# Kernel optimization log

Hardware: AMD Instinct MI355X
Metric: run time of the kernel (lower is better)

The kernel has to match this reference:

```python
import jax, jax.numpy as jnp
import numpy as np

BN_EPS = 1e-5
NN_EPS = 1e-8


def _three_nn_interp(xyz1, xyz2, points2):
    # xyz1: [B,N,3], xyz2: [B,S,3], points2: [B,S,D]
    # squared pairwise distances [B,N,S]
    d = (jnp.sum(xyz1 ** 2, -1)[:, :, None]
         + jnp.sum(xyz2 ** 2, -1)[:, None, :]
         - 2.0 * jnp.einsum('bnc,bsc->bns', xyz1, xyz2))
    neg_d3, idx = jax.lax.top_k(-d, 3)          # top-3 smallest dists
    d3 = -neg_d3                                # [B,N,3]
    recip = 1.0 / (d3 + NN_EPS)
    weight = recip / jnp.sum(recip, axis=2, keepdims=True)  # [B,N,3]
    gathered = jax.vmap(lambda p, i: p[i])(points2, idx)    # [B,N,3,D]
    return jnp.sum(gathered * weight[..., None], axis=2)    # [B,N,D]


def _conv_bn_relu(x, w, b, gamma, beta):
    # x: [B,C,N]; 1x1 conv == channel GEMM; BN in training mode (batch stats)
    y = jnp.einsum('oc,bcn->bon', w, x) + b[None, :, None]
    mean = jnp.mean(y, axis=(0, 2), keepdims=True)
    var = jnp.mean((y - mean) ** 2, axis=(0, 2), keepdims=True)
    y = (y - mean) * jax.lax.rsqrt(var + BN_EPS)
    y = y * gamma[None, :, None] + beta[None, :, None]
    return jax.nn.relu(y)


def setup_inputs() -> dict:
    key = jax.random.key(0)
    ks = jax.random.split(key, 8)
    B, N, S, D1, D2 = 8, 8192, 2048, 256, 256
    Cin, C0, C1 = D1 + D2, 256, 256
    return {
        'xyz1': jax.random.normal(ks[0], (B, 3, N), jnp.float32),
        'xyz2': jax.random.normal(ks[1], (B, 3, S), jnp.float32),
        'points1': jax.random.normal(ks[2], (B, D1, N), jnp.float32),
        'points2': jax.random.normal(ks[3], (B, D2, S), jnp.float32),
        'w0': jax.random.normal(ks[4], (C0, Cin), jnp.float32) * (1.0 / np.sqrt(Cin)),
        'b0': jnp.zeros((C0,), jnp.float32),
        'gamma0': jnp.ones((C0,), jnp.float32),
        'beta0': jnp.zeros((C0,), jnp.float32),
        'w1': jax.random.normal(ks[5], (C1, C0), jnp.float32) * (1.0 / np.sqrt(C0)),
        'b1': jnp.zeros((C1,), jnp.float32),
        'gamma1': jnp.ones((C1,), jnp.float32),
        'beta1': jnp.zeros((C1,), jnp.float32),
    }


def reference(xyz1, xyz2, points1, points2, w0, b0, gamma0, beta0, w1, b1, gamma1, beta1):
    x1 = jnp.transpose(xyz1, (0, 2, 1))     # [B,N,3]
    x2 = jnp.transpose(xyz2, (0, 2, 1))     # [B,S,3]
    p2 = jnp.transpose(points2, (0, 2, 1))  # [B,S,D2]
    interp = _three_nn_interp(x1, x2, p2)   # [B,N,D2]
    p1 = jnp.transpose(points1, (0, 2, 1))  # [B,N,D1]
    new_points = jnp.transpose(jnp.concatenate([p1, interp], axis=-1), (0, 2, 1))  # [B,Cin,N]
    h = _conv_bn_relu(new_points, w0, b0, gamma0, beta0)
    return _conv_bn_relu(h, w1, b1, gamma1, beta1)
```

## Files before the change

### kernel.cpp

```cpp
#include <hip/hip_runtime.h>
#include <math.h>

#define B 8
#define N 8192
#define S 2048
#define SCH 1024
#define C 256
#define CIN 512
#define CNT (B * N)
#define NSLOT 1024

typedef unsigned long long ull;
typedef __attribute__((ext_vector_type(8))) short bf16x8;
typedef __attribute__((ext_vector_type(4))) float floatx4;
typedef __attribute__((ext_vector_type(8))) unsigned short ushort8v;
typedef __attribute__((ext_vector_type(4))) unsigned short ushort4v;

__device__ inline unsigned short f2bf(float f) {
  unsigned u = __builtin_bit_cast(unsigned, f);
  u += 0x7FFF + ((u >> 16) & 1);
  return (unsigned short)(u >> 16);
}
__device__ inline float bf2f(unsigned short h) {
  unsigned u = ((unsigned)h) << 16;
  return __builtin_bit_cast(float, u);
}

__device__ inline void load_lds16(const void* g, void* l) {
  __builtin_amdgcn_global_load_lds(
      (const __attribute__((address_space(1))) unsigned int*)g,
      (__attribute__((address_space(3))) unsigned int*)l, 16, 0, 0);
}

__device__ inline void ins3u(ull k, ull& k0, ull& k1, ull& k2) {
  if (k < k2) {
    if (k < k1) {
      k2 = k1;
      if (k < k0) { k1 = k0; k0 = k; } else k1 = k;
    } else k2 = k;
  }
}

__device__ inline unsigned sortkey(float f) {
  unsigned u = __float_as_uint(f);
  return u ^ (((unsigned)((int)u >> 31)) | 0x80000000u);
}
__device__ inline float unsortkey(unsigned u) {
  unsigned m = ((int)u < 0) ? 0x80000000u : 0xFFFFFFFFu;
  return __uint_as_float(u ^ m);
}

__device__ inline void out3q(ull k0, ull k1, ull k2, float q2v,
                             int* __restrict__ idxbuf, float* __restrict__ wbuf,
                             size_t o) {
  float e0 = fmaxf(unsortkey((unsigned)(k0 >> 32)) + q2v, 0.0f);
  float e1 = fmaxf(unsortkey((unsigned)(k1 >> 32)) + q2v, 0.0f);
  float e2 = fmaxf(unsortkey((unsigned)(k2 >> 32)) + q2v, 0.0f);
  float r0 = 1.0f / (e0 + 1e-8f);
  float r1 = 1.0f / (e1 + 1e-8f);
  float r2 = 1.0f / (e2 + 1e-8f);
  float rs = 1.0f / (r0 + r1 + r2);
  idxbuf[o] = (int)(unsigned)k0;
  idxbuf[o + 1] = (int)(unsigned)k1;
  idxbuf[o + 2] = (int)(unsigned)k2;
  wbuf[o] = r0 * rs; wbuf[o + 1] = r1 * rs; wbuf[o + 2] = r2 * rs;
}

#define QDECL(q)                                                            \
  float d0_##q = INFINITY, d1_##q = INFINITY, d2_##q = INFINITY;            \
  int i0_##q = 0, i1_##q = 0, i2_##q = 0;                                   \
  float qx_##q, qy_##q, qz_##q, q2_##q;

#define QLOAD(q)                                                            \
  {                                                                         \
    float ox = p1[nq + q], oy = p1[N + nq + q], oz = p1[2 * N + nq + q];    \
    q2_##q = ox * ox + oy * oy + oz * oz;                                   \
    qx_##q = -2.0f * ox; qy_##q = -2.0f * oy; qz_##q = -2.0f * oz;          \
  }

#define QINS(q)                                                             \
  {                                                                         \
    float d = fmaf(qx_##q, pc.x, fmaf(qy_##q, pc.y, fmaf(qz_##q, pc.z, pc.w))); \
    bool lt0 = d < d0_##q, lt1 = d < d1_##q, lt2 = d < d2_##q;              \
    i2_##q = lt2 ? (lt1 ? i1_##q : s) : i2_##q;                             \
    i1_##q = lt1 ? (lt0 ? i0_##q : s) : i1_##q;                             \
    i0_##q = lt0 ? s : i0_##q;                                              \
    d2_##q = __builtin_amdgcn_fmed3f(d, d1_##q, d2_##q);                    \
    d1_##q = __builtin_amdgcn_fmed3f(d, d0_##q, d1_##q);                    \
    d0_##q = fminf(d, d0_##q);                                              \
  }

#define QSTORE(q)                                                           \
  {                                                                         \
    size_t kb = ((size_t)(grp * 2 + q) * 16 + sub) * 3;                     \
    keys[kb] = ((ull)sortkey(d0_##q) << 32) | (unsigned)i0_##q;             \
    keys[kb + 1] = ((ull)sortkey(d1_##q) << 32) | (unsigned)i1_##q;         \
    keys[kb + 2] = ((ull)sortkey(d2_##q) << 32) | (unsigned)i2_##q;         \
  }

__global__ __launch_bounds__(256, 4) void nn3_kernel(const float* __restrict__ xyz1,
                                                     const float* __restrict__ xyz2,
                                                     int* __restrict__ idxbuf,
                                                     float* __restrict__ wbuf) {
  __shared__ float4 sp[SCH];
  int b = blockIdx.x >> 8;
  int n0 = (blockIdx.x & 255) * 32;
  const float* p2 = xyz2 + (size_t)b * 3 * S;
  int tid = threadIdx.x;
  int sub = tid & 15, grp = tid >> 4;
  const float* p1 = xyz1 + (size_t)b * 3 * N;
  int nq = n0 + grp * 2;
  QDECL(0) QDECL(1)
  QLOAD(0) QLOAD(1)

  for (int ch = 0; ch < 2; ++ch) {
    if (ch) __syncthreads();
    for (int i = tid; i < SCH; i += 256) {
      int g = ch * SCH + i;
      float px = p2[g], py = p2[S + g], pz = p2[2 * S + g];
      sp[i] = make_float4(px, py, pz, px * px + py * py + pz * pz);
    }
    __syncthreads();
    int sbase = ch * SCH;
    float4 pc = sp[sub];
    for (int t = 0; t < SCH / 16 - 1; ++t) {
      float4 pn = sp[(t + 1) * 16 + sub];
      int s = sbase + t * 16 + sub;
      QINS(0) QINS(1)
      pc = pn;
    }
    {
      int s = sbase + SCH - 16 + sub;
      QINS(0) QINS(1)
    }
  }

  __syncthreads();
  ull* keys = (ull*)sp;
  QSTORE(0) QSTORE(1)
  __syncthreads();
  if (sub < 4) {
#pragma unroll
    for (int q = 0; q < 2; ++q) {
      size_t qb = (size_t)(grp * 2 + q) * 48;
      ull m0 = ~0ull, m1 = ~0ull, m2 = ~0ull;
#pragma unroll
      for (int jj = 0; jj < 4; ++jj) {
        size_t o2 = qb + (size_t)(sub + 4 * jj) * 3;
        ins3u(keys[o2], m0, m1, m2);
        ins3u(keys[o2 + 1], m0, m1, m2);
        ins3u(keys[o2 + 2], m0, m1, m2);
      }
#pragma unroll
      for (int mm = 1; mm <= 2; mm <<= 1) {
        ull e0 = (ull)__shfl_xor((long long)m0, mm);
        ull e1 = (ull)__shfl_xor((long long)m1, mm);
        ull e2 = (ull)__shfl_xor((long long)m2, mm);
        ins3u(e0, m0, m1, m2);
        ins3u(e1, m0, m1, m2);
        ins3u(e2, m0, m1, m2);
      }
      if (sub == 0) {
        float q2v = q ? q2_1 : q2_0;
        out3q(m0, m1, m2, q2v, idxbuf, wbuf, ((size_t)b * N + nq + q) * 3);
      }
    }
  }
}

__global__ __launch_bounds__(256) void convw_kernel(const float* __restrict__ w0,
                                                    const float* __restrict__ w1,
                                                    unsigned short* __restrict__ w0b,
                                                    unsigned short* __restrict__ w1b) {
  int i = blockIdx.x * 256 + threadIdx.x;
  if (i < C * CIN) w0b[i] = f2bf(w0[i]);
  else {
    int j = i - C * CIN;
    if (j < C * C) w1b[j] = f2bf(w1[j]);
  }
}

__global__ __launch_bounds__(256) void tconv_kernel(const float* __restrict__ src,
                                                    unsigned short* __restrict__ dst,
                                                    int cols, int drow, int coff) {
  __shared__ float t[64][65];
  int n0 = blockIdx.x * 64, c0 = blockIdx.y * 64, b = blockIdx.z;
  int tid = threadIdx.x, r = tid >> 2, q = tid & 3;
  const float* sp = src + ((size_t)b * 256 + c0 + r) * cols + n0 + q * 16;
#pragma unroll
  for (int i = 0; i < 4; ++i) {
    float4 v = *(const float4*)(sp + i * 4);
    t[r][q * 16 + i * 4 + 0] = v.x;
    t[r][q * 16 + i * 4 + 1] = v.y;
    t[r][q * 16 + i * 4 + 2] = v.z;
    t[r][q * 16 + i * 4 + 3] = v.w;
  }
  __syncthreads();
  unsigned short* dp = dst + ((size_t)b * cols + n0 + r) * drow + coff + c0 + q * 16;
  ushort8v o0, o1;
#pragma unroll
  for (int i = 0; i < 8; ++i) o0[i] = f2bf(t[q * 16 + i][r]);
#pragma unroll
  for (int i = 0; i < 8; ++i) o1[i] = f2bf(t[q * 16 + 8 + i][r]);
  *(ushort8v*)dp = o0;
  *(ushort8v*)(dp + 8) = o1;
}

__global__ __launch_bounds__(256) void gather_kernel(const unsigned short* __restrict__ p2t,
                                                     const int* __restrict__ idxbuf,
                                                     const float* __restrict__ wbuf,
                                                     unsigned short* __restrict__ Xb) {
  __shared__ int si[192];
  __shared__ float sw[192];
  int b = blockIdx.x >> 7;
  int n0 = (blockIdx.x & 127) * 64;
  size_t base = ((size_t)b * N + n0) * 3;
  if (threadIdx.x < 192) {
    si[threadIdx.x] = idxbuf[base + threadIdx.x];
    sw[threadIdx.x] = wbuf[base + threadIdx.x];
  }
  __syncthreads();
  int nl = threadIdx.x >> 2, cb = threadIdx.x & 3;
  int j0 = si[nl * 3], j1 = si[nl * 3 + 1], j2 = si[nl * 3 + 2];
  float w0 = sw[nl * 3], w1 = sw[nl * 3 + 1], w2 = sw[nl * 3 + 2];
  const unsigned short* pb = p2t + (size_t)b * S * 256;
  const unsigned short* r0p = pb + (size_t)j0 * 256;
  const unsigned short* r1p = pb + (size_t)j1 * 256;
  const unsigned short* r2p = pb + (size_t)j2 * 256;
  unsigned short* xp = Xb + ((size_t)b * N + n0 + nl) * 512 + 256;
#pragma unroll
  for (int ch = 0; ch < 8; ++ch) {
    int co = (cb + ch * 4) * 8;
    ushort8v v0 = *(const ushort8v*)(r0p + co);
    ushort8v v1 = *(const ushort8v*)(r1p + co);
    ushort8v v2 = *(const ushort8v*)(r2p + co);
    ushort8v o;
#pragma unroll
    for (int i = 0; i < 8; ++i)
      o[i] = f2bf(w0 * bf2f(v0[i]) + w1 * bf2f(v1[i]) + w2 * bf2f(v2[i]));
    *(ushort8v*)(xp + co) = o;
  }
}

__global__ __launch_bounds__(256) void gemm_kernel(const unsigned short* __restrict__ X,
                                                   const unsigned short* __restrict__ Wb,
                                                   const float* __restrict__ bias,
                                                   unsigned short* __restrict__ Y,
                                                   float* __restrict__ psum,
                                                   float* __restrict__ psumsq,
                                                   int Cin) {
  __shared__ unsigned short As[128 * 32];
  __shared__ unsigned short Bs[128 * 32];
  int n0 = blockIdx.x * 128, o0 = blockIdx.y * 128, b = blockIdx.z;
  int tid = threadIdx.x, lane = tid & 63, wid = tid >> 6;
  int wm = wid >> 1, wn = wid & 1;
  floatx4 acc[4][4];
#pragma unroll
  for (int m = 0; m < 4; ++m)
#pragma unroll
    for (int nt = 0; nt < 4; ++nt) acc[m][nt] = (floatx4)(0.0f);

  size_t rsA = (size_t)Cin * 2;
  int chunkSwz = ((lane & 3) ^ ((lane >> 3) & 3)) * 16;
  const char* Abase = (const char*)Wb + (size_t)(o0 + wid * 32 + (lane >> 2)) * rsA + chunkSwz;
  const char* Bbase = (const char*)X + ((size_t)b * N + n0 + wid * 32 + (lane >> 2)) * rsA + chunkSwz;
  size_t rstep16 = 16 * rsA;
  int kq = (((lane >> 4) ^ ((lane >> 1) & 3))) * 8;

  for (int k0 = 0; k0 < Cin; k0 += 32) {
    load_lds16(Abase + (size_t)k0 * 2, &As[(wid * 32) * 32]);
    load_lds16(Abase + (size_t)k0 * 2 + rstep16, &As[(wid * 32 + 16) * 32]);
    load_lds16(Bbase + (size_t)k0 * 2, &Bs[(wid * 32) * 32]);
    load_lds16(Bbase + (size_t)k0 * 2 + rstep16, &Bs[(wid * 32 + 16) * 32]);
    __syncthreads();
    bf16x8 af[4], bfv[4];
#pragma unroll
    for (int m = 0; m < 4; ++m)
      af[m] = *(const bf16x8*)&As[(wm * 64 + m * 16 + (lane & 15)) * 32 + kq];
#pragma unroll
    for (int nt = 0; nt < 4; ++nt)
      bfv[nt] = *(const bf16x8*)&Bs[(wn * 64 + nt * 16 + (lane & 15)) * 32 + kq];
#pragma unroll
    for (int m = 0; m < 4; ++m)
#pragma unroll
      for (int nt = 0; nt < 4; ++nt)
        acc[m][nt] = __builtin_amdgcn_mfma_f32_16x16x32_bf16(af[m], bfv[nt], acc[m][nt], 0, 0, 0);
    __syncthreads();
  }

  int col = lane & 15, rowq = lane >> 4;
  int slot = ((b * 64 + blockIdx.x) * 2) + wn;
#pragma unroll
  for (int m = 0; m < 4; ++m) {
    int ob = o0 + wm * 64 + m * 16 + rowq * 4;
    float4 bs = *(const float4*)&bias[ob];
    float sj[4] = {0.f, 0.f, 0.f, 0.f}, qj[4] = {0.f, 0.f, 0.f, 0.f};
#pragma unroll
    for (int nt = 0; nt < 4; ++nt) {
      int n = n0 + wn * 64 + nt * 16 + col;
      float y0 = acc[m][nt][0] + bs.x;
      float y1 = acc[m][nt][1] + bs.y;
      float y2 = acc[m][nt][2] + bs.z;
      float y3 = acc[m][nt][3] + bs.w;
      ushort4v v;
      v[0] = f2bf(y0); v[1] = f2bf(y1); v[2] = f2bf(y2); v[3] = f2bf(y3);
      *(ushort4v*)&Y[((size_t)b * N + n) * 256 + ob] = v;
      sj[0] += y0; qj[0] = fmaf(y0, y0, qj[0]);
      sj[1] += y1; qj[1] = fmaf(y1, y1, qj[1]);
      sj[2] += y2; qj[2] = fmaf(y2, y2, qj[2]);
      sj[3] += y3; qj[3] = fmaf(y3, y3, qj[3]);
    }
#pragma unroll
    for (int j = 0; j < 4; ++j) {
#pragma unroll
      for (int d = 1; d <= 8; d <<= 1) {
        sj[j] += __shfl_xor(sj[j], d);
        qj[j] += __shfl_xor(qj[j], d);
      }
    }
    if (col == 0) {
      int c0 = blockIdx.y * 128 + wm * 64 + m * 16 + rowq * 4;
#pragma unroll
      for (int j = 0; j < 4; ++j) {
        psum[(size_t)(c0 + j) * NSLOT + slot] = sj[j];
        psumsq[(size_t)(c0 + j) * NSLOT + slot] = qj[j];
      }
    }
  }
}

__global__ __launch_bounds__(256) void bnparam_kernel(const float* __restrict__ psum,
                                                      const float* __restrict__ psumsq,
                                                      const float* __restrict__ gamma,
                                                      const float* __restrict__ beta,
                                                      float* __restrict__ scale,
                                                      float* __restrict__ shift) {
  int c = blockIdx.x, tid = threadIdx.x;
  const float* ps = psum + (size_t)c * NSLOT;
  const float* pq = psumsq + (size_t)c * NSLOT;
  float s = 0.f, q = 0.f;
#pragma unroll
  for (int i = 0; i < NSLOT / 256; ++i) {
    s += ps[tid + i * 256];
    q += pq[tid + i * 256];
  }
#pragma unroll
  for (int d = 1; d <= 32; d <<= 1) {
    s += __shfl_xor(s, d);
    q += __shfl_xor(q, d);
  }
  __shared__ float ls[4], lq[4];
  int wid = tid >> 6;
  if ((tid & 63) == 0) { ls[wid] = s; lq[wid] = q; }
  __syncthreads();
  if (tid == 0) {
    s = ls[0] + ls[1] + ls[2] + ls[3];
    q = lq[0] + lq[1] + lq[2] + lq[3];
    float m = s * (1.0f / CNT);
    float v = q * (1.0f / CNT) - m * m;
    float sc = gamma[c] * rsqrtf(v + 1e-5f);
    scale[c] = sc;
    shift[c] = beta[c] - m * sc;
  }
}

__global__ __launch_bounds__(256) void bnrelu_kernel(const unsigned short* __restrict__ Y,
                                                     const float* __restrict__ scale,
                                                     const float* __restrict__ shift,
                                                     unsigned short* __restrict__ H) {
  size_t total = (size_t)B * N * 256 / 8;
  for (size_t i = (size_t)blockIdx.x * 256 + threadIdx.x; i < total;
       i += (size_t)gridDim.x * 256) {
    int ob = ((int)i & 31) * 8;
    float4 s0 = *(const float4*)&scale[ob];
    float4 s1 = *(const float4*)&scale[ob + 4];
    float4 h0 = *(const float4*)&shift[ob];
    float4 h1 = *(const float4*)&shift[ob + 4];
    ushort8v v = *(const ushort8v*)&Y[i * 8];
    ushort8v o;
    o[0] = f2bf(fmaxf(fmaf(bf2f(v[0]), s0.x, h0.x), 0.f));
    o[1] = f2bf(fmaxf(fmaf(bf2f(v[1]), s0.y, h0.y), 0.f));
    o[2] = f2bf(fmaxf(fmaf(bf2f(v[2]), s0.z, h0.z), 0.f));
    o[3] = f2bf(fmaxf(fmaf(bf2f(v[3]), s0.w, h0.w), 0.f));
    o[4] = f2bf(fmaxf(fmaf(bf2f(v[4]), s1.x, h1.x), 0.f));
    o[5] = f2bf(fmaxf(fmaf(bf2f(v[5]), s1.y, h1.y), 0.f));
    o[6] = f2bf(fmaxf(fmaf(bf2f(v[6]), s1.z, h1.z), 0.f));
    o[7] = f2bf(fmaxf(fmaf(bf2f(v[7]), s1.w, h1.w), 0.f));
    *(ushort8v*)&H[i * 8] = o;
  }
}

__global__ __launch_bounds__(256) void bnreluT_kernel(const unsigned short* __restrict__ Y,
                                                      const float* __restrict__ scale,
                                                      const float* __restrict__ shift,
                                                      float* __restrict__ out) {
  __shared__ float t[64][65];
  int n0 = blockIdx.x * 64, o0 = blockIdx.y * 64, b = blockIdx.z;
  int tid = threadIdx.x, r = tid >> 2, q = tid & 3;
  const unsigned short* yp = Y + ((size_t)b * N + n0 + r) * 256 + o0 + q * 16;
#pragma unroll
  for (int h = 0; h < 2; ++h) {
    ushort8v v = *(const ushort8v*)(yp + h * 8);
#pragma unroll
    for (int i = 0; i < 8; ++i) {
      int oc = q * 16 + h * 8 + i;
      float f = fmaxf(fmaf(bf2f(v[i]), scale[o0 + oc], shift[o0 + oc]), 0.f);
      t[oc][r] = f;
    }
  }
  __syncthreads();
  float* op = out + ((size_t)b * 256 + o0 + r) * N + n0 + q * 16;
#pragma unroll
  for (int i = 0; i < 4; ++i) {
    float4 v = make_float4(t[r][q * 16 + i * 4 + 0], t[r][q * 16 + i * 4 + 1],
                           t[r][q * 16 + i * 4 + 2], t[r][q * 16 + i * 4 + 3]);
    *(float4*)(op + i * 4) = v;
  }
}

extern "C" void kernel_launch(void* const* d_in, const int* in_sizes, int n_in,
                              void* d_out, int out_size, void* d_ws, size_t ws_size,
                              hipStream_t stream) {
  const float* xyz1 = (const float*)d_in[0];
  const float* xyz2 = (const float*)d_in[1];
  const float* points1 = (const float*)d_in[2];
  const float* points2 = (const float*)d_in[3];
  const float* w0 = (const float*)d_in[4];
  const float* b0 = (const float*)d_in[5];
  const float* g0 = (const float*)d_in[6];
  const float* be0 = (const float*)d_in[7];
  const float* w1 = (const float*)d_in[8];
  const float* b1 = (const float*)d_in[9];
  const float* g1 = (const float*)d_in[10];
  const float* be1 = (const float*)d_in[11];
  float* out = (float*)d_out;

  char* ws = (char*)d_ws;
  int* idxbuf = (int*)ws;              ws += (size_t)CNT * 3 * 4;
  float* wbuf = (float*)ws;            ws += (size_t)CNT * 3 * 4;
  float* scale0 = (float*)ws;          ws += 256 * 4;
  float* shift0 = (float*)ws;          ws += 256 * 4;
  float* scale1 = (float*)ws;          ws += 256 * 4;
  float* shift1 = (float*)ws;          ws += 256 * 4;
  float* psum = (float*)ws;            ws += (size_t)C * NSLOT * 4;
  float* psumsq = (float*)ws;          ws += (size_t)C * NSLOT * 4;
  unsigned short* w0b = (unsigned short*)ws;  ws += (size_t)C * CIN * 2;
  unsigned short* w1b = (unsigned short*)ws;  ws += (size_t)C * C * 2;
  unsigned short* p2t = (unsigned short*)ws;  ws += (size_t)B * S * 256 * 2;
  unsigned short* Xb = (unsigned short*)ws;   ws += (size_t)B * N * 512 * 2;
  unsigned short* Yb = (unsigned short*)ws;   ws += (size_t)B * N * 256 * 2;
  unsigned short* Hb = Xb;

  convw_kernel<<<dim3((C * CIN + C * C) / 256), 256, 0, stream>>>(w0, w1, w0b, w1b);
  tconv_kernel<<<dim3(N / 64, 4, B), 256, 0, stream>>>(points1, Xb, N, 512, 0);
  tconv_kernel<<<dim3(S / 64, 4, B), 256, 0, stream>>>(points2, p2t, S, 256, 0);
  nn3_kernel<<<dim3(B * N / 32), 256, 0, stream>>>(xyz1, xyz2, idxbuf, wbuf);
  gather_kernel<<<dim3(B * N / 64), 256, 0, stream>>>(p2t, idxbuf, wbuf, Xb);
  gemm_kernel<<<dim3(N / 128, 2, B), 256, 0, stream>>>(Xb, w0b, b0, Yb, psum, psumsq, CIN);
  bnparam_kernel<<<dim3(C), 256, 0, stream>>>(psum, psumsq, g0, be0, scale0, shift0);
  bnrelu_kernel<<<dim3(2048), 256, 0, stream>>>(Yb, scale0, shift0, Hb);
  gemm_kernel<<<dim3(N / 128, 2, B), 256, 0, stream>>>(Hb, w1b, b1, Yb, psum, psumsq, C);
  bnparam_kernel<<<dim3(C), 256, 0, stream>>>(psum, psumsq, g1, be1, scale1, shift1);
  bnreluT_kernel<<<dim3(N / 64, 4, B), 256, 0, stream>>>(Yb, scale1, shift1, out);
}
```

Baseline: 229.9 us.

## Merge prep kernels into one launch and unroll NN candidate loop by two

The weight conversion kernel and the two transpose-convert kernels become a single prep kernel that dispatches on block index, saving two launches and letting their blocks share the GPU. Separately, the three-nearest-neighbour scan loop is unrolled by two, with two LDS candidates prefetched per iteration, to expose more instruction-level parallelism. The unroll raises register pressure in nn3, and the merged kernel must route block indices correctly.

```diff
diff --git a/kernel.cpp b/kernel.cpp
--- a/kernel.cpp
+++ b/kernel.cpp
@@ -122,15 +122,33 @@
     }
     __syncthreads();
     int sbase = ch * SCH;
-    float4 pc = sp[sub];
-    for (int t = 0; t < SCH / 16 - 1; ++t) {
-      float4 pn = sp[(t + 1) * 16 + sub];
-      int s = sbase + t * 16 + sub;
+    const float4* spp = sp + sub;
+    float4 pcA = spp[0];
+    float4 pcB = spp[16];
+    for (int t = 0; t < SCH / 16 - 2; t += 2) {
+      float4 pnA = spp[(t + 2) * 16];
+      float4 pnB = spp[(t + 3) * 16];
+      {
+        float4 pc = pcA;
+        int s = sbase + t * 16 + sub;
+        QINS(0) QINS(1)
+      }
+      {
+        float4 pc = pcB;
+        int s = sbase + (t + 1) * 16 + sub;
+        QINS(0) QINS(1)
+      }
+      pcA = pnA;
+      pcB = pnB;
+    }
+    {
+      float4 pc = pcA;
+      int s = sbase + (SCH / 16 - 2) * 16 + sub;
       QINS(0) QINS(1)
-      pc = pn;
     }
     {
-      int s = sbase + SCH - 16 + sub;
+      float4 pc = pcB;
+      int s = sbase + (SCH / 16 - 1) * 16 + sub;
       QINS(0) QINS(1)
     }
   }
@@ -168,23 +186,11 @@
   }
 }
 
-__global__ __launch_bounds__(256) void convw_kernel(const float* __restrict__ w0,
-                                                    const float* __restrict__ w1,
-                                                    unsigned short* __restrict__ w0b,
-                                                    unsigned short* __restrict__ w1b) {
-  int i = blockIdx.x * 256 + threadIdx.x;
-  if (i < C * CIN) w0b[i] = f2bf(w0[i]);
-  else {
-    int j = i - C * CIN;
-    if (j < C * C) w1b[j] = f2bf(w1[j]);
-  }
-}
-
-__global__ __launch_bounds__(256) void tconv_kernel(const float* __restrict__ src,
-                                                    unsigned short* __restrict__ dst,
-                                                    int cols, int drow, int coff) {
-  __shared__ float t[64][65];
-  int n0 = blockIdx.x * 64, c0 = blockIdx.y * 64, b = blockIdx.z;
+__device__ inline void tconv_body(const float* __restrict__ src,
+                                  unsigned short* __restrict__ dst,
+                                  int cols, int drow, int bx, int by, int bz,
+                                  float (*t)[65]) {
+  int n0 = bx * 64, c0 = by * 64, b = bz;
   int tid = threadIdx.x, r = tid >> 2, q = tid & 3;
   const float* sp = src + ((size_t)b * 256 + c0 + r) * cols + n0 + q * 16;
 #pragma unroll
@@ -196,7 +202,7 @@
     t[r][q * 16 + i * 4 + 3] = v.w;
   }
   __syncthreads();
-  unsigned short* dp = dst + ((size_t)b * cols + n0 + r) * drow + coff + c0 + q * 16;
+  unsigned short* dp = dst + ((size_t)b * cols + n0 + r) * drow + c0 + q * 16;
   ushort8v o0, o1;
 #pragma unroll
   for (int i = 0; i < 8; ++i) o0[i] = f2bf(t[q * 16 + i][r]);
@@ -204,6 +210,31 @@
   for (int i = 0; i < 8; ++i) o1[i] = f2bf(t[q * 16 + 8 + i][r]);
   *(ushort8v*)dp = o0;
   *(ushort8v*)(dp + 8) = o1;
+}
+
+__global__ __launch_bounds__(256) void prep_kernel(const float* __restrict__ points1,
+                                                   const float* __restrict__ points2,
+                                                   const float* __restrict__ w0,
+                                                   const float* __restrict__ w1,
+                                                   unsigned short* __restrict__ Xb,
+                                                   unsigned short* __restrict__ p2t,
+                                                   unsigned short* __restrict__ w0b,
+                                                   unsigned short* __restrict__ w1b) {
+  __shared__ float t[64][65];
+  int id = blockIdx.x;
+  if (id < 4096) {
+    tconv_body(points1, Xb, N, 512, id & 127, (id >> 7) & 3, id >> 9, t);
+  } else if (id < 5120) {
+    id -= 4096;
+    tconv_body(points2, p2t, S, 256, id & 31, (id >> 5) & 3, id >> 7, t);
+  } else {
+    int i = (id - 5120) * 256 + threadIdx.x;
+    if (i < C * CIN) w0b[i] = f2bf(w0[i]);
+    else {
+      int j = i - C * CIN;
+      if (j < C * C) w1b[j] = f2bf(w1[j]);
+    }
+  }
 }
 
 __global__ __launch_bounds__(256) void gather_kernel(const unsigned short* __restrict__ p2t,
@@ -451,9 +482,8 @@
   unsigned short* Yb = (unsigned short*)ws;   ws += (size_t)B * N * 256 * 2;
   unsigned short* Hb = Xb;
 
-  convw_kernel<<<dim3((C * CIN + C * C) / 256), 256, 0, stream>>>(w0, w1, w0b, w1b);
-  tconv_kernel<<<dim3(N / 64, 4, B), 256, 0, stream>>>(points1, Xb, N, 512, 0);
-  tconv_kernel<<<dim3(S / 64, 4, B), 256, 0, stream>>>(points2, p2t, S, 256, 0);
+  prep_kernel<<<dim3(4096 + 1024 + 768), 256, 0, stream>>>(points1, points2, w0, w1,
+                                                           Xb, p2t, w0b, w1b);
   nn3_kernel<<<dim3(B * N / 32), 256, 0, stream>>>(xyz1, xyz2, idxbuf, wbuf);
   gather_kernel<<<dim3(B * N / 64), 256, 0, stream>>>(p2t, idxbuf, wbuf, Xb);
   gemm_kernel<<<dim3(N / 128, 2, B), 256, 0, stream>>>(Xb, w0b, b0, Yb, psum, psumsq, CIN);
```

After: 223.8 us. -2.7%, faster.
